# Performance work log

Measured on AMD Instinct MI355X. Metric: run time of the kernel, lower is better.

Reference implementation:

```python
import jax, jax.numpy as jnp
import numpy as np

B, T, F_, H, HEADS = 16, 64, 64, 64, 4
D = H // HEADS            # per-head out dim (rnn_hidden // heads)
DEG = 16                  # avg degree of random feature graph
NEG_SLOPE = 0.2           # DGL GATConv default leaky_relu slope


def setup_inputs() -> dict:
    key = jax.random.key(0)
    ks = jax.random.split(key, 10)
    rng = np.random.default_rng(0)
    src_r = rng.integers(0, F_, size=F_ * DEG)
    dst_r = rng.integers(0, F_, size=F_ * DEG)
    loops = np.arange(F_)  # dgl.add_self_loop
    src = jnp.asarray(np.concatenate([src_r, loops]), jnp.int32)
    dst = jnp.asarray(np.concatenate([dst_r, loops]), jnp.int32)
    s = lambda k, shape, sc: (jax.random.normal(k, shape, jnp.float32) * sc)
    return {
        "history_stack": jax.random.normal(ks[0], (B, T, F_), jnp.float32),
        "src": src,
        "dst": dst,
        "W_enc": s(ks[1], (F_, H), 0.5),           # per-feature Linear(1, H) weights
        "b_enc": s(ks[2], (F_, H), 0.1),
        "W_gat": s(ks[3], (H, HEADS * D), 0.1),    # GATConv fc (no bias)
        "attn_l": s(ks[4], (HEADS, D), 0.1),
        "attn_r": s(ks[5], (HEADS, D), 0.1),
        "b_gat": jnp.zeros((HEADS * D,), jnp.float32),
        "W_ih": s(ks[6], (F_, 3 * H, H), 0.1),     # per-feature GRU params (r,z,n order)
        "W_hh": s(ks[7], (F_, 3 * H, H), 0.1),
        "b_ih": jnp.zeros((F_, 3 * H), jnp.float32),
        "b_hh": jnp.zeros((F_, 3 * H), jnp.float32),
        "W_dec": s(ks[8], (F_, H), 0.1),           # per-feature Linear(H, 1)
        "b_dec": s(ks[9], (F_,), 0.1),
    }


def _gat(x, src, dst, W_gat, attn_l, attn_r, b_gat):
    # x: [BT, N, H] -> [BT, N, H]; same graph replicated over leading axis.
    BT, N, _ = x.shape
    feat = (x @ W_gat).reshape(BT, N, HEADS, D)
    el = jnp.einsum('bnhd,hd->bnh', feat, attn_l)
    er = jnp.einsum('bnhd,hd->bnh', feat, attn_r)
    e = jax.nn.leaky_relu(el[:, src] + er[:, dst], NEG_SLOPE)  # [BT, E, HEADS]

    def softmax_agg(e_b, feat_b):
        m = jax.ops.segment_max(e_b, dst, num_segments=N)      # per-dst max
        ex = jnp.exp(e_b - m[dst])
        den = jax.ops.segment_sum(ex, dst, num_segments=N)
        alpha = ex / den[dst]                                   # [E, HEADS]
        msg = alpha[..., None] * feat_b[src]                    # [E, HEADS, D]
        return jax.ops.segment_sum(msg, dst, num_segments=N)   # [N, HEADS, D]

    out = jax.vmap(softmax_agg)(e, feat)
    return out.reshape(BT, N, HEADS * D) + b_gat


def _gru(x, Wih, Whh, bih, bhh):
    # x: [T, B, H]; torch GRU cell with zero initial state, gate order r,z,n.
    xW = x @ Wih.T + bih  # precompute input projections: [T, B, 3H]

    def step(h, xw):
        hW = h @ Whh.T + bhh
        xr, xz, xn = jnp.split(xw, 3, -1)
        hr, hz, hn = jnp.split(hW, 3, -1)
        r = jax.nn.sigmoid(xr + hr)
        z = jax.nn.sigmoid(xz + hz)
        n = jnp.tanh(xn + r * hn)
        h_new = (1.0 - z) * n + z * h
        return h_new, h_new

    h0 = jnp.zeros((x.shape[1], x.shape[2]), x.dtype)
    _, hs = jax.lax.scan(step, h0, xW)
    return hs  # [T, B, H]


def reference(history_stack, src, dst, W_enc, b_enc, W_gat, attn_l, attn_r,
              b_gat, W_ih, W_hh, b_ih, b_hh, W_dec, b_dec):
    Bb, Tt, Ff = history_stack.shape
    # per-feature encoders: Linear(1, H) -> [B, T, F, H]
    enc = jnp.einsum('btf,fh->btfh', history_stack, W_enc) + b_enc
    x = enc.reshape(Bb * Tt, Ff, -1)
    g = _gat(x, src, dst, W_gat, attn_l, attn_r, b_gat).reshape(Bb, Tt, Ff, -1)
    # per-feature GRUs over time: vmap over F of scan over T
    xf = jnp.transpose(g, (2, 1, 0, 3))                 # [F, T, B, H]
    hs = jax.vmap(_gru)(xf, W_ih, W_hh, b_ih, b_hh)     # [F, T, B, H]
    hiddens = jnp.transpose(hs, (2, 1, 0, 3))           # [B, T, F, H]
    # per-feature decoders: Linear(H, 1), squeezed
    ans = jnp.einsum('btfh,fh->btf', hiddens, W_dec) + b_dec
    return ans, hiddens
```

## Files before the change

kernel.cpp:

```cpp
#include <hip/hip_runtime.h>
#include <hip/hip_bf16.h>
#include <math.h>

#define Bb 16
#define Tt 64
#define Ff 64
#define MAXE 2048

typedef __fp16 h2f __attribute__((ext_vector_type(2)));
__device__ __forceinline__ h2f pkh(float a, float b) {
  return __builtin_amdgcn_cvt_pkrtz(a, b);
}

__global__ __launch_bounds__(256) void kprep(
    const int* __restrict__ src, const int* __restrict__ dst, int E,
    const float* __restrict__ W_enc, const float* __restrict__ b_enc,
    const float* __restrict__ W_gat, const float* __restrict__ attn_l,
    const float* __restrict__ attn_r, const float* __restrict__ b_gat,
    int* __restrict__ off, int* __restrict__ csr,
    float* __restrict__ A, float* __restrict__ Bc,
    float* __restrict__ aA, float* __restrict__ aB,
    float* __restrict__ rA, float* __restrict__ rB) {
  __shared__ int s_src[MAXE], s_dst[MAXE];
  __shared__ int cnt[Ff], base[Ff];
  __shared__ __align__(16) float We[64][64], Be[64][64], Wg[64][64];
  __shared__ __align__(16) float As[64][64], Bs[64][64];
  __shared__ float al_s[64], ar_s[64], bg_s[64];
  int t = threadIdx.x;

  if (blockIdx.x == 0) {
    for (int e = t; e < E; e += 256) { s_src[e] = src[e]; s_dst[e] = dst[e]; }
    if (t < Ff) cnt[t] = 0;
    __syncthreads();
    for (int e = t; e < E; e += 256) atomicAdd(&cnt[s_dst[e]], 1);
    __syncthreads();
    if (t < 64) {
      int c = cnt[t];
      int inc = c;
#pragma unroll
      for (int ofs = 1; ofs < 64; ofs <<= 1) {
        int up = __shfl_up(inc, ofs, 64);
        if (t >= ofs) inc += up;
      }
      int exc = inc - c;
      off[t] = exc;
      base[t] = exc;
      if (t == 63) off[64] = inc;
      for (int chunk = 0; chunk < E; chunk += 64) {
        int e = chunk + t;
        bool valid = e < E;
        int di = valid ? s_dst[e] : 64;
        unsigned long long m = ~0ull;
#pragma unroll
        for (int bnum = 0; bnum < 7; ++bnum) {
          unsigned long long bb = __ballot((di >> bnum) & 1);
          m &= ((di >> bnum) & 1) ? bb : ~bb;
        }
        unsigned long long below = m & ((1ull << t) - 1ull);
        int rank = __popcll(below);
        if (valid) {
          int slot = base[di] + rank;
          csr[slot] = s_src[e];
          if (below == 0ull) base[di] += __popcll(m);
        }
      }
    }
    return;
  }

  for (int i = t; i < 1024; i += 256) {
    ((float4*)We)[i] = ((const float4*)W_enc)[i];
    ((float4*)Be)[i] = ((const float4*)b_enc)[i];
    ((float4*)Wg)[i] = ((const float4*)W_gat)[i];
  }
  if (t < 64) { al_s[t] = attn_l[t]; ar_s[t] = attn_r[t]; bg_s[t] = b_gat[t]; }
  __syncthreads();
  int n = t >> 2, q = t & 3;
  float accA[16], accB[16];
#pragma unroll
  for (int j = 0; j < 16; ++j) { accA[j] = 0.f; accB[j] = 0.f; }
  for (int k = 0; k < 64; ++k) {
    float we = We[n][k], be = Be[n][k];
#pragma unroll
    for (int c = 0; c < 4; ++c) {
      float4 wg = *(const float4*)&Wg[k][q * 16 + c * 4];
      accA[c*4+0] = fmaf(we, wg.x, accA[c*4+0]); accB[c*4+0] = fmaf(be, wg.x, accB[c*4+0]);
      accA[c*4+1] = fmaf(we, wg.y, accA[c*4+1]); accB[c*4+1] = fmaf(be, wg.y, accB[c*4+1]);
      accA[c*4+2] = fmaf(we, wg.z, accA[c*4+2]); accB[c*4+2] = fmaf(be, wg.z, accB[c*4+2]);
      accA[c*4+3] = fmaf(we, wg.w, accA[c*4+3]); accB[c*4+3] = fmaf(be, wg.w, accB[c*4+3]);
    }
  }
#pragma unroll
  for (int c = 0; c < 4; ++c) {
    float4 va, vb, vbg;
    va.x = accA[c*4+0]; va.y = accA[c*4+1]; va.z = accA[c*4+2]; va.w = accA[c*4+3];
    vb.x = accB[c*4+0]; vb.y = accB[c*4+1]; vb.z = accB[c*4+2]; vb.w = accB[c*4+3];
    vbg.x = vb.x + bg_s[q*16+c*4+0]; vbg.y = vb.y + bg_s[q*16+c*4+1];
    vbg.z = vb.z + bg_s[q*16+c*4+2]; vbg.w = vb.w + bg_s[q*16+c*4+3];
    *(float4*)&As[n][q*16 + c*4] = va;
    *(float4*)&Bs[n][q*16 + c*4] = vb;
    *(float4*)&A[n*64 + q*16 + c*4] = va;
    *(float4*)&Bc[n*64 + q*16 + c*4] = vbg;
  }
  __syncthreads();
  float sa = 0.f, sb = 0.f, sra = 0.f, srb = 0.f;
#pragma unroll
  for (int j = 0; j < 16; ++j) {
    float alv = al_s[q*16 + j], arv = ar_s[q*16 + j];
    float av = As[n][q*16 + j], bv = Bs[n][q*16 + j];
    sa  = fmaf(av, alv, sa);  sb  = fmaf(bv, alv, sb);
    sra = fmaf(av, arv, sra); srb = fmaf(bv, arv, srb);
  }
  aA[t] = sa; aB[t] = sb; rA[t] = sra; rB[t] = srb;
}

__global__ __launch_bounds__(256) void k_gat(
    const float* __restrict__ hist, const float* __restrict__ Ag,
    const float* __restrict__ Bg, const float* __restrict__ aAg,
    const float* __restrict__ aBg, const float* __restrict__ rAg,
    const float* __restrict__ rBg, const int* __restrict__ off,
    const int* __restrict__ csr, int E, float* __restrict__ g_out) {
  __shared__ __align__(16) float feat[64 * 68];
  __shared__ float x_s[64];
  __shared__ float el_s[64][4], er_s[64][4];
  __shared__ int csr_s[1152];
  __shared__ int off_s[Ff + 1];
  int bt = blockIdx.x, t = threadIdx.x;
  if (t < 64) x_s[t] = hist[bt * 64 + t];
  if (t < Ff + 1) off_s[t] = off[t];
  for (int e = t; e < E; e += 256) csr_s[e] = csr[e];
  __syncthreads();

  int s0 = t >> 2, q = t & 3;
  {
    float xs = x_s[s0];
    const float4* Ar = (const float4*)(Ag + (s0 << 6) + (q << 4));
    const float4* Br = (const float4*)(Bg + (s0 << 6) + (q << 4));
#pragma unroll
    for (int c = 0; c < 4; ++c) {
      float4 a4 = Ar[c], b4 = Br[c];
      float4 o;
      o.x = fmaf(xs, a4.x, b4.x); o.y = fmaf(xs, a4.y, b4.y);
      o.z = fmaf(xs, a4.z, b4.z); o.w = fmaf(xs, a4.w, b4.w);
      *(float4*)&feat[s0 * 68 + (q << 4) + (c << 2)] = o;
    }
    el_s[s0][q] = fmaf(xs, aAg[t], aBg[t]);
    er_s[s0][q] = fmaf(xs, rAg[t], rBg[t]);
  }
  __syncthreads();

  int d = s0, hd = q;
  int o0 = off_s[d], o1 = off_s[d + 1];
  float erd = er_s[d][hd];
  float den = 0.f;
  float acc[16];
#pragma unroll
  for (int j = 0; j < 16; ++j) acc[j] = 0.f;
  for (int e = o0; e < o1; ++e) {
    int s = csr_s[e];
    float ee = el_s[s][hd] + erd;
    ee = fmaxf(ee, 0.2f * ee);
    float p = __expf(ee);
    den += p;
    const float* fr = &feat[s * 68 + (hd << 4)];
#pragma unroll
    for (int c = 0; c < 4; ++c) {
      float4 fv = *(const float4*)&fr[c << 2];
      acc[c*4+0] = fmaf(p, fv.x, acc[c*4+0]);
      acc[c*4+1] = fmaf(p, fv.y, acc[c*4+1]);
      acc[c*4+2] = fmaf(p, fv.z, acc[c*4+2]);
      acc[c*4+3] = fmaf(p, fv.w, acc[c*4+3]);
    }
  }
  float inv = __builtin_amdgcn_rcpf(den);
  float* gp = g_out + (size_t)bt * 4096 + (d << 6) + (hd << 4);
#pragma unroll
  for (int c = 0; c < 4; ++c) {
    float4 o;
    o.x = acc[c*4+0] * inv; o.y = acc[c*4+1] * inv;
    o.z = acc[c*4+2] * inv; o.w = acc[c*4+3] * inv;
    *(float4*)&gp[c << 2] = o;
  }
}

__device__ __forceinline__ float qsum(float v) {
  v += __int_as_float(__builtin_amdgcn_mov_dpp(__float_as_int(v), 0xB1, 0xF, 0xF, true));
  v += __int_as_float(__builtin_amdgcn_mov_dpp(__float_as_int(v), 0x4E, 0xF, 0xF, true));
  return v;
}

__global__ __launch_bounds__(256, 4) void k_gru(
    const float* __restrict__ W_ih, const float* __restrict__ W_hh,
    const float* __restrict__ b_ih, const float* __restrict__ b_hh,
    const float* __restrict__ W_dec, const float* __restrict__ b_dec,
    float* __restrict__ hid, float* __restrict__ ans) {
  __shared__ __align__(16) h2f g16[16][32];
  __shared__ __align__(16) float4 xw4[16 * 64];
  __shared__ __align__(16) __fp16 h16[2][64];
  __shared__ __align__(16) float hbuf[2][8][64];
  int blk = blockIdx.x;
  int f = blk & 63, b = blk >> 6;
  int t = threadIdx.x;
  int row = t >> 2, kg = t & 3;

  const float* Wi = W_ih + f * 12288 + (kg << 4);
  const float* Wh = W_hh + f * 12288 + (kg << 4);
  h2f wi0[8], wi1[8], wi2[8], wh0[8], wh1[8], wh2[8];
#pragma unroll
  for (int c = 0; c < 4; ++c) {
    float4 v;
    v = *(const float4*)(Wi + (row << 6)         + (c << 2));
    wi0[c*2] = pkh(v.x, v.y); wi0[c*2+1] = pkh(v.z, v.w);
    v = *(const float4*)(Wi + ((64 + row) << 6)  + (c << 2));
    wi1[c*2] = pkh(v.x, v.y); wi1[c*2+1] = pkh(v.z, v.w);
    v = *(const float4*)(Wi + ((128 + row) << 6) + (c << 2));
    wi2[c*2] = pkh(v.x, v.y); wi2[c*2+1] = pkh(v.z, v.w);
    v = *(const float4*)(Wh + (row << 6)         + (c << 2));
    wh0[c*2] = pkh(v.x, v.y); wh0[c*2+1] = pkh(v.z, v.w);
    v = *(const float4*)(Wh + ((64 + row) << 6)  + (c << 2));
    wh1[c*2] = pkh(v.x, v.y); wh1[c*2+1] = pkh(v.z, v.w);
    v = *(const float4*)(Wh + ((128 + row) << 6) + (c << 2));
    wh2[c*2] = pkh(v.x, v.y); wh2[c*2+1] = pkh(v.z, v.w);
  }
  float bR  = b_ih[f*192 + row]       + b_hh[f*192 + row];
  float bZ  = b_ih[f*192 + 64 + row]  + b_hh[f*192 + 64 + row];
  float bXN = b_ih[f*192 + 128 + row];
  float bHN = b_hh[f*192 + 128 + row];
  int j2 = t & 31;
  float wd0 = W_dec[(f << 6) + j2], wd1 = W_dec[(f << 6) + 32 + j2];
  float bdec = b_dec[f];
  size_t hidbase = (size_t)b * 262144 + (f << 6);
  float hreg = 0.f;
  if (t < 64) { h16[0][t] = (__fp16)0.f; h16[1][t] = (__fp16)0.f; }
  __syncthreads();

#pragma unroll 1
  for (int G = 0; G < 4; ++G) {
    {
      int i = t >> 4, ch = t & 15;
      float4 v = *(const float4*)&hid[hidbase + (size_t)((G << 4) + i) * 4096 + (ch << 2)];
      g16[i][(ch << 1)]     = pkh(v.x, v.y);
      g16[i][(ch << 1) + 1] = pkh(v.z, v.w);
    }
    __syncthreads();

#pragma unroll
    for (int ts = 0; ts < 16; ++ts) {
      const h2f* gp = &g16[ts][kg << 3];
      h2f gv[8];
#pragma unroll
      for (int j = 0; j < 8; ++j) gv[j] = gp[j];
      float p0 = 0.f, p1 = 0.f, p2 = 0.f;
#pragma unroll
      for (int j = 0; j < 8; ++j) {
        p0 = __builtin_amdgcn_fdot2(gv[j], wi0[j], p0, false);
        p1 = __builtin_amdgcn_fdot2(gv[j], wi1[j], p1, false);
        p2 = __builtin_amdgcn_fdot2(gv[j], wi2[j], p2, false);
      }
      p0 = qsum(p0); p1 = qsum(p1); p2 = qsum(p2);
      if (kg == 0) {
        float4 o; o.x = p0; o.y = p1; o.z = p2; o.w = 0.f;
        xw4[(ts << 6) + row] = o;
      }
    }

#pragma unroll
    for (int st = 0; st < 16; ++st) {
      const int cur = st & 1;
      float4 xg = xw4[(st << 6) + row];
      const h2f* hp = (const h2f*)&h16[cur][kg << 4];
      h2f hv[8];
#pragma unroll
      for (int j = 0; j < 8; ++j) hv[j] = hp[j];
      float pr = 0.f, pz = 0.f, pn = 0.f;
#pragma unroll
      for (int j = 0; j < 8; ++j) {
        pr = __builtin_amdgcn_fdot2(hv[j], wh0[j], pr, false);
        pz = __builtin_amdgcn_fdot2(hv[j], wh1[j], pz, false);
        pn = __builtin_amdgcn_fdot2(hv[j], wh2[j], pn, false);
      }
      pr = qsum(pr); pz = qsum(pz); pn = qsum(pn);
      float rr = __builtin_amdgcn_rcpf(1.f + __expf(-(pr + xg.x + bR)));
      float zz = __builtin_amdgcn_rcpf(1.f + __expf(-(pz + xg.y + bZ)));
      float pre = fmaf(rr, pn + bHN, xg.z + bXN);
      float nn = 1.f - 2.f * __builtin_amdgcn_rcpf(1.f + __expf(2.f * pre));
      float hnew = fmaf(zz, hreg - nn, nn);
      hreg = hnew;
      if (kg == 0) h16[cur ^ 1][row] = (__fp16)hnew;
      if (kg == 1) hbuf[(st >> 3) & 1][st & 7][row] = hnew;
      __syncthreads();
      if ((st & 7) == 7) {
        const int gsel = (st >> 3) & 1;
        int ts0 = (G << 4) + st - 7;
        if (t < 128) {
          int i = t >> 4, j = t & 15;
          float4 hv4 = *(const float4*)&hbuf[gsel][i][j << 2];
          *(float4*)&hid[hidbase + (size_t)(ts0 + i) * 4096 + (j << 2)] = hv4;
        }
        int i2 = t >> 5;
        float part = hbuf[gsel][i2][j2] * wd0 + hbuf[gsel][i2][j2 + 32] * wd1;
        part += __shfl_xor(part, 1);  part += __shfl_xor(part, 2);
        part += __shfl_xor(part, 4);  part += __shfl_xor(part, 8);
        part += __shfl_xor(part, 16);
        if (j2 == 0) ans[((b << 6) + ts0 + i2) * 64 + f] = part + bdec;
      }
    }
  }
}

extern "C" void kernel_launch(void* const* d_in, const int* in_sizes, int n_in,
                              void* d_out, int out_size, void* d_ws, size_t ws_size,
                              hipStream_t stream) {
  const float* hist   = (const float*)d_in[0];
  const int* src      = (const int*)d_in[1];
  const int* dst      = (const int*)d_in[2];
  const float* W_enc  = (const float*)d_in[3];
  const float* b_enc  = (const float*)d_in[4];
  const float* W_gat  = (const float*)d_in[5];
  const float* attn_l = (const float*)d_in[6];
  const float* attn_r = (const float*)d_in[7];
  const float* b_gat  = (const float*)d_in[8];
  const float* W_ih   = (const float*)d_in[9];
  const float* W_hh   = (const float*)d_in[10];
  const float* b_ih   = (const float*)d_in[11];
  const float* b_hh   = (const float*)d_in[12];
  const float* W_dec  = (const float*)d_in[13];
  const float* b_dec  = (const float*)d_in[14];
  int E = in_sizes[1];

  float* ans = (float*)d_out;
  float* hid = (float*)d_out + Bb * Tt * Ff;

  int* off   = (int*)d_ws;
  int* csr   = off + 256;
  float* A   = (float*)(csr + 2048);
  float* Bc  = A + 4096;
  float* aA  = Bc + 4096;
  float* aB  = aA + 256;
  float* rA  = aB + 256;
  float* rB  = rA + 256;

  hipLaunchKernelGGL(kprep, dim3(2), dim3(256), 0, stream,
                     src, dst, E, W_enc, b_enc, W_gat, attn_l, attn_r, b_gat,
                     off, csr, A, Bc, aA, aB, rA, rB);
  hipLaunchKernelGGL(k_gat, dim3(Bb * Tt), dim3(256), 0, stream,
                     hist, A, Bc, aA, aB, rA, rB, off, csr, E, hid);
  hipLaunchKernelGGL(k_gru, dim3(Ff * Bb), dim3(256), 0, stream,
                     W_ih, W_hh, b_ih, b_hh, W_dec, b_dec, hid, ans);
}
```

Baseline: 94.49 us.

## Process two batch elements per GRU block to share register-held weights

Each k_gru block now runs the recurrence for two batch elements of the same feature instead of one, interleaving their dot products and sharing the packed fp16 weights held in registers. This halves the grid, halves the weight loads per batch element, and gives each sequential step two independent dependency chains for latency hiding. In exchange register and LDS use roughly double, launch bounds drop from 4 to 3 blocks per SM, and only 512 blocks remain, which lowers parallelism across the device.

```diff
diff --git a/kernel.cpp b/kernel.cpp
--- a/kernel.cpp
+++ b/kernel.cpp
@@ -189,17 +189,18 @@
   return v;
 }
 
-__global__ __launch_bounds__(256, 4) void k_gru(
+__global__ __launch_bounds__(256, 3) void k_gru(
     const float* __restrict__ W_ih, const float* __restrict__ W_hh,
     const float* __restrict__ b_ih, const float* __restrict__ b_hh,
     const float* __restrict__ W_dec, const float* __restrict__ b_dec,
     float* __restrict__ hid, float* __restrict__ ans) {
-  __shared__ __align__(16) h2f g16[16][32];
-  __shared__ __align__(16) float4 xw4[16 * 64];
-  __shared__ __align__(16) __fp16 h16[2][64];
-  __shared__ __align__(16) float hbuf[2][8][64];
+  __shared__ __align__(16) h2f g16[2][16][32];
+  __shared__ __align__(16) float4 xw4[2][16 * 64];
+  __shared__ __align__(16) __fp16 h16[2][2][64];
+  __shared__ __align__(16) float hbuf[2][2][8][64];
   int blk = blockIdx.x;
-  int f = blk & 63, b = blk >> 6;
+  int f = blk & 63, bg = blk >> 6;
+  int bA = bg << 1, bB = bA + 1;
   int t = threadIdx.x;
   int row = t >> 2, kg = t & 3;
 
@@ -229,80 +230,121 @@
   int j2 = t & 31;
   float wd0 = W_dec[(f << 6) + j2], wd1 = W_dec[(f << 6) + 32 + j2];
   float bdec = b_dec[f];
-  size_t hidbase = (size_t)b * 262144 + (f << 6);
-  float hreg = 0.f;
-  if (t < 64) { h16[0][t] = (__fp16)0.f; h16[1][t] = (__fp16)0.f; }
+  size_t baseA = (size_t)bA * 262144 + (f << 6);
+  size_t baseB = (size_t)bB * 262144 + (f << 6);
+  float hregA = 0.f, hregB = 0.f;
+  if (t < 64) {
+    h16[0][0][t] = (__fp16)0.f; h16[0][1][t] = (__fp16)0.f;
+    h16[1][0][t] = (__fp16)0.f; h16[1][1][t] = (__fp16)0.f;
+  }
   __syncthreads();
 
 #pragma unroll 1
   for (int G = 0; G < 4; ++G) {
-    {
-      int i = t >> 4, ch = t & 15;
-      float4 v = *(const float4*)&hid[hidbase + (size_t)((G << 4) + i) * 4096 + (ch << 2)];
-      g16[i][(ch << 1)]     = pkh(v.x, v.y);
-      g16[i][(ch << 1) + 1] = pkh(v.z, v.w);
+#pragma unroll
+    for (int r = 0; r < 2; ++r) {
+      int idx = r * 256 + t;
+      int bb = idx >> 8, rem = idx & 255;
+      int i = rem >> 4, ch = rem & 15;
+      size_t base = bb ? baseB : baseA;
+      float4 v = *(const float4*)&hid[base + (size_t)((G << 4) + i) * 4096 + (ch << 2)];
+      g16[bb][i][(ch << 1)]     = pkh(v.x, v.y);
+      g16[bb][i][(ch << 1) + 1] = pkh(v.z, v.w);
     }
     __syncthreads();
 
 #pragma unroll
     for (int ts = 0; ts < 16; ++ts) {
-      const h2f* gp = &g16[ts][kg << 3];
-      h2f gv[8];
-#pragma unroll
-      for (int j = 0; j < 8; ++j) gv[j] = gp[j];
-      float p0 = 0.f, p1 = 0.f, p2 = 0.f;
+      const h2f* gpA = &g16[0][ts][kg << 3];
+      const h2f* gpB = &g16[1][ts][kg << 3];
+      h2f gvA[8], gvB[8];
+#pragma unroll
+      for (int j = 0; j < 8; ++j) { gvA[j] = gpA[j]; gvB[j] = gpB[j]; }
+      float a0 = 0.f, a1 = 0.f, a2 = 0.f, b0 = 0.f, b1 = 0.f, b2 = 0.f;
 #pragma unroll
       for (int j = 0; j < 8; ++j) {
-        p0 = __builtin_amdgcn_fdot2(gv[j], wi0[j], p0, false);
-        p1 = __builtin_amdgcn_fdot2(gv[j], wi1[j], p1, false);
-        p2 = __builtin_amdgcn_fdot2(gv[j], wi2[j], p2, false);
-      }
-      p0 = qsum(p0); p1 = qsum(p1); p2 = qsum(p2);
+        a0 = __builtin_amdgcn_fdot2(gvA[j], wi0[j], a0, false);
+        b0 = __builtin_amdgcn_fdot2(gvB[j], wi0[j], b0, false);
+        a1 = __builtin_amdgcn_fdot2(gvA[j], wi1[j], a1, false);
+        b1 = __builtin_amdgcn_fdot2(gvB[j], wi1[j], b1, false);
+        a2 = __builtin_amdgcn_fdot2(gvA[j], wi2[j], a2, false);
+        b2 = __builtin_amdgcn_fdot2(gvB[j], wi2[j], b2, false);
+      }
+      a0 = qsum(a0); b0 = qsum(b0); a1 = qsum(a1);
+      b1 = qsum(b1); a2 = qsum(a2); b2 = qsum(b2);
       if (kg == 0) {
-        float4 o; o.x = p0; o.y = p1; o.z = p2; o.w = 0.f;
-        xw4[(ts << 6) + row] = o;
+        float4 oa; oa.x = a0; oa.y = a1; oa.z = a2; oa.w = 0.f;
+        float4 ob; ob.x = b0; ob.y = b1; ob.z = b2; ob.w = 0.f;
+        xw4[0][(ts << 6) + row] = oa;
+        xw4[1][(ts << 6) + row] = ob;
       }
     }
 
 #pragma unroll
     for (int st = 0; st < 16; ++st) {
       const int cur = st & 1;
-      float4 xg = xw4[(st << 6) + row];
-      const h2f* hp = (const h2f*)&h16[cur][kg << 4];
-      h2f hv[8];
-#pragma unroll
-      for (int j = 0; j < 8; ++j) hv[j] = hp[j];
-      float pr = 0.f, pz = 0.f, pn = 0.f;
+      float4 xgA = xw4[0][(st << 6) + row];
+      float4 xgB = xw4[1][(st << 6) + row];
+      const h2f* hpA = (const h2f*)&h16[0][cur][kg << 4];
+      const h2f* hpB = (const h2f*)&h16[1][cur][kg << 4];
+      h2f hvA[8], hvB[8];
+#pragma unroll
+      for (int j = 0; j < 8; ++j) { hvA[j] = hpA[j]; hvB[j] = hpB[j]; }
+      float prA = 0.f, pzA = 0.f, pnA = 0.f;
+      float prB = 0.f, pzB = 0.f, pnB = 0.f;
 #pragma unroll
       for (int j = 0; j < 8; ++j) {
-        pr = __builtin_amdgcn_fdot2(hv[j], wh0[j], pr, false);
-        pz = __builtin_amdgcn_fdot2(hv[j], wh1[j], pz, false);
-        pn = __builtin_amdgcn_fdot2(hv[j], wh2[j], pn, false);
-      }
-      pr = qsum(pr); pz = qsum(pz); pn = qsum(pn);
-      float rr = __builtin_amdgcn_rcpf(1.f + __expf(-(pr + xg.x + bR)));
-      float zz = __builtin_amdgcn_rcpf(1.f + __expf(-(pz + xg.y + bZ)));
-      float pre = fmaf(rr, pn + bHN, xg.z + bXN);
-      float nn = 1.f - 2.f * __builtin_amdgcn_rcpf(1.f + __expf(2.f * pre));
-      float hnew = fmaf(zz, hreg - nn, nn);
-      hreg = hnew;
-      if (kg == 0) h16[cur ^ 1][row] = (__fp16)hnew;
-      if (kg == 1) hbuf[(st >> 3) & 1][st & 7][row] = hnew;
+        prA = __builtin_amdgcn_fdot2(hvA[j], wh0[j], prA, false);
+        prB = __builtin_amdgcn_fdot2(hvB[j], wh0[j], prB, false);
+        pzA = __builtin_amdgcn_fdot2(hvA[j], wh1[j], pzA, false);
+        pzB = __builtin_amdgcn_fdot2(hvB[j], wh1[j], pzB, false);
+        pnA = __builtin_amdgcn_fdot2(hvA[j], wh2[j], pnA, false);
+        pnB = __builtin_amdgcn_fdot2(hvB[j], wh2[j], pnB, false);
+      }
+      prA = qsum(prA); prB = qsum(prB); pzA = qsum(pzA);
+      pzB = qsum(pzB); pnA = qsum(pnA); pnB = qsum(pnB);
+      float rrA = __builtin_amdgcn_rcpf(1.f + __expf(-(prA + xgA.x + bR)));
+      float rrB = __builtin_amdgcn_rcpf(1.f + __expf(-(prB + xgB.x + bR)));
+      float zzA = __builtin_amdgcn_rcpf(1.f + __expf(-(pzA + xgA.y + bZ)));
+      float zzB = __builtin_amdgcn_rcpf(1.f + __expf(-(pzB + xgB.y + bZ)));
+      float preA = fmaf(rrA, pnA + bHN, xgA.z + bXN);
+      float preB = fmaf(rrB, pnB + bHN, xgB.z + bXN);
+      float nnA = 1.f - 2.f * __builtin_amdgcn_rcpf(1.f + __expf(2.f * preA));
+      float nnB = 1.f - 2.f * __builtin_amdgcn_rcpf(1.f + __expf(2.f * preB));
+      float hnA = fmaf(zzA, hregA - nnA, nnA);
+      float hnB = fmaf(zzB, hregB - nnB, nnB);
+      hregA = hnA; hregB = hnB;
+      if (kg == 0) {
+        h16[0][cur ^ 1][row] = (__fp16)hnA;
+        h16[1][cur ^ 1][row] = (__fp16)hnB;
+      }
+      if (kg == 1) {
+        hbuf[0][(st >> 3) & 1][st & 7][row] = hnA;
+        hbuf[1][(st >> 3) & 1][st & 7][row] = hnB;
+      }
       __syncthreads();
       if ((st & 7) == 7) {
         const int gsel = (st >> 3) & 1;
         int ts0 = (G << 4) + st - 7;
-        if (t < 128) {
-          int i = t >> 4, j = t & 15;
-          float4 hv4 = *(const float4*)&hbuf[gsel][i][j << 2];
-          *(float4*)&hid[hidbase + (size_t)(ts0 + i) * 4096 + (j << 2)] = hv4;
+        {
+          int half = t >> 7, tt = t & 127;
+          int i = tt >> 4, j = tt & 15;
+          float4 hv4 = *(const float4*)&hbuf[half][gsel][i][j << 2];
+          size_t base = half ? baseB : baseA;
+          *(float4*)&hid[base + (size_t)(ts0 + i) * 4096 + (j << 2)] = hv4;
         }
         int i2 = t >> 5;
-        float part = hbuf[gsel][i2][j2] * wd0 + hbuf[gsel][i2][j2 + 32] * wd1;
-        part += __shfl_xor(part, 1);  part += __shfl_xor(part, 2);
-        part += __shfl_xor(part, 4);  part += __shfl_xor(part, 8);
-        part += __shfl_xor(part, 16);
-        if (j2 == 0) ans[((b << 6) + ts0 + i2) * 64 + f] = part + bdec;
+        float pa = hbuf[0][gsel][i2][j2] * wd0 + hbuf[0][gsel][i2][j2 + 32] * wd1;
+        float pb = hbuf[1][gsel][i2][j2] * wd0 + hbuf[1][gsel][i2][j2 + 32] * wd1;
+        pa += __shfl_xor(pa, 1);  pb += __shfl_xor(pb, 1);
+        pa += __shfl_xor(pa, 2);  pb += __shfl_xor(pb, 2);
+        pa += __shfl_xor(pa, 4);  pb += __shfl_xor(pb, 4);
+        pa += __shfl_xor(pa, 8);  pb += __shfl_xor(pb, 8);
+        pa += __shfl_xor(pa, 16); pb += __shfl_xor(pb, 16);
+        if (j2 == 0) {
+          ans[((bA << 6) + ts0 + i2) * 64 + f] = pa + bdec;
+          ans[((bB << 6) + ts0 + i2) * 64 + f] = pb + bdec;
+        }
       }
     }
   }
@@ -345,6 +387,6 @@
                      off, csr, A, Bc, aA, aB, rA, rB);
   hipLaunchKernelGGL(k_gat, dim3(Bb * Tt), dim3(256), 0, stream,
                      hist, A, Bc, aA, aB, rA, rB, off, csr, E, hid);
-  hipLaunchKernelGGL(k_gru, dim3(Ff * Bb), dim3(256), 0, stream,
+  hipLaunchKernelGGL(k_gru, dim3(Ff * Bb / 2), dim3(256), 0, stream,
                      W_ih, W_hh, b_ih, b_hh, W_dec, b_dec, hid, ans);
 }
```

Result: slower. 97.81 us (+3.5%).

## Restructure GRU kernel to one wavefront per sequence with full-row weights in registers

Applied to the files above, without the earlier changes.

The GRU kernel now uses a single 64-thread wavefront per (batch, feature) sequence. Each thread holds its full 64-wide weight rows for all six gate matrices in registers as packed fp16, and the whole 64-step GAT input is staged into LDS once. This removes the cross-lane quad reductions, the separate input-projection phase and the chunked buffering of hidden outputs. In exchange it needs 192 packed registers of weights per thread, which risks spills or very low occupancy, and each step runs a longer serial dot-product chain with scalar hidden-state stores.

```diff
diff --git a/kernel.cpp b/kernel.cpp
--- a/kernel.cpp
+++ b/kernel.cpp
@@ -183,128 +183,89 @@
   }
 }
 
-__device__ __forceinline__ float qsum(float v) {
-  v += __int_as_float(__builtin_amdgcn_mov_dpp(__float_as_int(v), 0xB1, 0xF, 0xF, true));
-  v += __int_as_float(__builtin_amdgcn_mov_dpp(__float_as_int(v), 0x4E, 0xF, 0xF, true));
-  return v;
-}
-
-__global__ __launch_bounds__(256, 4) void k_gru(
+__global__ __launch_bounds__(64, 1) void k_gru(
     const float* __restrict__ W_ih, const float* __restrict__ W_hh,
     const float* __restrict__ b_ih, const float* __restrict__ b_hh,
     const float* __restrict__ W_dec, const float* __restrict__ b_dec,
     float* __restrict__ hid, float* __restrict__ ans) {
-  __shared__ __align__(16) h2f g16[16][32];
-  __shared__ __align__(16) float4 xw4[16 * 64];
-  __shared__ __align__(16) __fp16 h16[2][64];
-  __shared__ __align__(16) float hbuf[2][8][64];
+  __shared__ __align__(16) h2f gall[64][32];
+  __shared__ __align__(16) __fp16 h16[64];
   int blk = blockIdx.x;
   int f = blk & 63, b = blk >> 6;
   int t = threadIdx.x;
-  int row = t >> 2, kg = t & 3;
-
-  const float* Wi = W_ih + f * 12288 + (kg << 4);
-  const float* Wh = W_hh + f * 12288 + (kg << 4);
-  h2f wi0[8], wi1[8], wi2[8], wh0[8], wh1[8], wh2[8];
-#pragma unroll
-  for (int c = 0; c < 4; ++c) {
+
+  const float* WiB = W_ih + f * 12288 + (t << 6);
+  const float* WhB = W_hh + f * 12288 + (t << 6);
+  h2f wi0[32], wi1[32], wi2[32], wh0[32], wh1[32], wh2[32];
+#pragma unroll
+  for (int c = 0; c < 16; ++c) {
     float4 v;
-    v = *(const float4*)(Wi + (row << 6)         + (c << 2));
+    v = *(const float4*)(WiB + (c << 2));
     wi0[c*2] = pkh(v.x, v.y); wi0[c*2+1] = pkh(v.z, v.w);
-    v = *(const float4*)(Wi + ((64 + row) << 6)  + (c << 2));
+    v = *(const float4*)(WiB + 4096 + (c << 2));
     wi1[c*2] = pkh(v.x, v.y); wi1[c*2+1] = pkh(v.z, v.w);
-    v = *(const float4*)(Wi + ((128 + row) << 6) + (c << 2));
+    v = *(const float4*)(WiB + 8192 + (c << 2));
     wi2[c*2] = pkh(v.x, v.y); wi2[c*2+1] = pkh(v.z, v.w);
-    v = *(const float4*)(Wh + (row << 6)         + (c << 2));
+    v = *(const float4*)(WhB + (c << 2));
     wh0[c*2] = pkh(v.x, v.y); wh0[c*2+1] = pkh(v.z, v.w);
-    v = *(const float4*)(Wh + ((64 + row) << 6)  + (c << 2));
+    v = *(const float4*)(WhB + 4096 + (c << 2));
     wh1[c*2] = pkh(v.x, v.y); wh1[c*2+1] = pkh(v.z, v.w);
-    v = *(const float4*)(Wh + ((128 + row) << 6) + (c << 2));
+    v = *(const float4*)(WhB + 8192 + (c << 2));
     wh2[c*2] = pkh(v.x, v.y); wh2[c*2+1] = pkh(v.z, v.w);
   }
-  float bR  = b_ih[f*192 + row]       + b_hh[f*192 + row];
-  float bZ  = b_ih[f*192 + 64 + row]  + b_hh[f*192 + 64 + row];
-  float bXN = b_ih[f*192 + 128 + row];
-  float bHN = b_hh[f*192 + 128 + row];
-  int j2 = t & 31;
-  float wd0 = W_dec[(f << 6) + j2], wd1 = W_dec[(f << 6) + 32 + j2];
+  float bR  = b_ih[f*192 + t]       + b_hh[f*192 + t];
+  float bZ  = b_ih[f*192 + 64 + t]  + b_hh[f*192 + 64 + t];
+  float bXN = b_ih[f*192 + 128 + t];
+  float bHN = b_hh[f*192 + 128 + t];
+  float wd   = W_dec[(f << 6) + t];
   float bdec = b_dec[f];
-  size_t hidbase = (size_t)b * 262144 + (f << 6);
+  size_t base = (size_t)b * 262144 + (f << 6);
+
+#pragma unroll
+  for (int c = 0; c < 16; ++c) {
+    float4 v = *(const float4*)&hid[base + (size_t)t * 4096 + (c << 2)];
+    gall[t][c*2]     = pkh(v.x, v.y);
+    gall[t][c*2+1]   = pkh(v.z, v.w);
+  }
+  h16[t] = (__fp16)0.f;
+  __syncthreads();
+
   float hreg = 0.f;
-  if (t < 64) { h16[0][t] = (__fp16)0.f; h16[1][t] = (__fp16)0.f; }
-  __syncthreads();
-
-#pragma unroll 1
-  for (int G = 0; G < 4; ++G) {
-    {
-      int i = t >> 4, ch = t & 15;
-      float4 v = *(const float4*)&hid[hidbase + (size_t)((G << 4) + i) * 4096 + (ch << 2)];
-      g16[i][(ch << 1)]     = pkh(v.x, v.y);
-      g16[i][(ch << 1) + 1] = pkh(v.z, v.w);
-    }
+#pragma unroll 4
+  for (int ts = 0; ts < 64; ++ts) {
+    h2f gv[32], hv[32];
+#pragma unroll
+    for (int j = 0; j < 8; ++j) {
+      *(float4*)&gv[j*4] = *(const float4*)&gall[ts][j*4];
+      *(float4*)&hv[j*4] = *(const float4*)&h16[j*8];
+    }
+    float p0 = 0.f, p1 = 0.f, p2 = 0.f, q0 = 0.f, q1 = 0.f, q2 = 0.f;
+#pragma unroll
+    for (int j = 0; j < 32; ++j) {
+      p0 = __builtin_amdgcn_fdot2(gv[j], wi0[j], p0, false);
+      q0 = __builtin_amdgcn_fdot2(hv[j], wh0[j], q0, false);
+      p1 = __builtin_amdgcn_fdot2(gv[j], wi1[j], p1, false);
+      q1 = __builtin_amdgcn_fdot2(hv[j], wh1[j], q1, false);
+      p2 = __builtin_amdgcn_fdot2(gv[j], wi2[j], p2, false);
+      q2 = __builtin_amdgcn_fdot2(hv[j], wh2[j], q2, false);
+    }
+    float rr = __builtin_amdgcn_rcpf(1.f + __expf(-(p0 + q0 + bR)));
+    float zz = __builtin_amdgcn_rcpf(1.f + __expf(-(p1 + q1 + bZ)));
+    float pre = fmaf(rr, q2 + bHN, p2 + bXN);
+    float nn = 1.f - 2.f * __builtin_amdgcn_rcpf(1.f + __expf(2.f * pre));
+    float hnew = fmaf(zz, hreg - nn, nn);
+    hreg = hnew;
+    h16[t] = (__fp16)hnew;
+    hid[base + (size_t)ts * 4096 + t] = hnew;
+    float part = hnew * wd;
+    part += __shfl_xor(part, 1);
+    part += __shfl_xor(part, 2);
+    part += __shfl_xor(part, 4);
+    part += __shfl_xor(part, 8);
+    part += __shfl_xor(part, 16);
+    part += __shfl_xor(part, 32);
+    if (t == 0) ans[(((b << 6) + ts) << 6) + f] = part + bdec;
     __syncthreads();
-
-#pragma unroll
-    for (int ts = 0; ts < 16; ++ts) {
-      const h2f* gp = &g16[ts][kg << 3];
-      h2f gv[8];
-#pragma unroll
-      for (int j = 0; j < 8; ++j) gv[j] = gp[j];
-      float p0 = 0.f, p1 = 0.f, p2 = 0.f;
-#pragma unroll
-      for (int j = 0; j < 8; ++j) {
-        p0 = __builtin_amdgcn_fdot2(gv[j], wi0[j], p0, false);
-        p1 = __builtin_amdgcn_fdot2(gv[j], wi1[j], p1, false);
-        p2 = __builtin_amdgcn_fdot2(gv[j], wi2[j], p2, false);
-      }
-      p0 = qsum(p0); p1 = qsum(p1); p2 = qsum(p2);
-      if (kg == 0) {
-        float4 o; o.x = p0; o.y = p1; o.z = p2; o.w = 0.f;
-        xw4[(ts << 6) + row] = o;
-      }
-    }
-
-#pragma unroll
-    for (int st = 0; st < 16; ++st) {
-      const int cur = st & 1;
-      float4 xg = xw4[(st << 6) + row];
-      const h2f* hp = (const h2f*)&h16[cur][kg << 4];
-      h2f hv[8];
-#pragma unroll
-      for (int j = 0; j < 8; ++j) hv[j] = hp[j];
-      float pr = 0.f, pz = 0.f, pn = 0.f;
-#pragma unroll
-      for (int j = 0; j < 8; ++j) {
-        pr = __builtin_amdgcn_fdot2(hv[j], wh0[j], pr, false);
-        pz = __builtin_amdgcn_fdot2(hv[j], wh1[j], pz, false);
-        pn = __builtin_amdgcn_fdot2(hv[j], wh2[j], pn, false);
-      }
-      pr = qsum(pr); pz = qsum(pz); pn = qsum(pn);
-      float rr = __builtin_amdgcn_rcpf(1.f + __expf(-(pr + xg.x + bR)));
-      float zz = __builtin_amdgcn_rcpf(1.f + __expf(-(pz + xg.y + bZ)));
-      float pre = fmaf(rr, pn + bHN, xg.z + bXN);
-      float nn = 1.f - 2.f * __builtin_amdgcn_rcpf(1.f + __expf(2.f * pre));
-      float hnew = fmaf(zz, hreg - nn, nn);
-      hreg = hnew;
-      if (kg == 0) h16[cur ^ 1][row] = (__fp16)hnew;
-      if (kg == 1) hbuf[(st >> 3) & 1][st & 7][row] = hnew;
-      __syncthreads();
-      if ((st & 7) == 7) {
-        const int gsel = (st >> 3) & 1;
-        int ts0 = (G << 4) + st - 7;
-        if (t < 128) {
-          int i = t >> 4, j = t & 15;
-          float4 hv4 = *(const float4*)&hbuf[gsel][i][j << 2];
-          *(float4*)&hid[hidbase + (size_t)(ts0 + i) * 4096 + (j << 2)] = hv4;
-        }
-        int i2 = t >> 5;
-        float part = hbuf[gsel][i2][j2] * wd0 + hbuf[gsel][i2][j2 + 32] * wd1;
-        part += __shfl_xor(part, 1);  part += __shfl_xor(part, 2);
-        part += __shfl_xor(part, 4);  part += __shfl_xor(part, 8);
-        part += __shfl_xor(part, 16);
-        if (j2 == 0) ans[((b << 6) + ts0 + i2) * 64 + f] = part + bdec;
-      }
-    }
   }
 }
 
@@ -345,6 +306,6 @@
                      off, csr, A, Bc, aA, aB, rA, rB);
   hipLaunchKernelGGL(k_gat, dim3(Bb * Tt), dim3(256), 0, stream,
                      hist, A, Bc, aA, aB, rA, rB, off, csr, E, hid);
-  hipLaunchKernelGGL(k_gru, dim3(Ff * Bb), dim3(256), 0, stream,
+  hipLaunchKernelGGL(k_gru, dim3(Ff * Bb), dim3(64), 0, stream,
                      W_ih, W_hh, b_ih, b_hh, W_dec, b_dec, hid, ans);
 }
```

New measurement: 93.17 us. About the same (-1.4%).
